# Kernel tuning notes

Hardware: AMD Instinct MI355X
Metric: run time of the kernel (lower is better)

The kernel has to match this reference:

```python
import jax, jax.numpy as jnp
import numpy as np

B, H, IN, OUT, T = 1024, 1024, 512, 8192, 15
EPS = 1e-5


def setup_inputs() -> dict:
    key = jax.random.key(0)
    ks = jax.random.split(key, 20)
    s = 0.02
    d = {
        'z': jax.random.normal(ks[0], (B, H), jnp.float32),
        'input_length': T,
        # ConvTranspose1d weights, torch layout [in, out, k] == jax 'IOH'
        'cw1': jax.random.normal(ks[1], (H, H, 3), jnp.float32) * s,
        'cb1': jax.random.normal(ks[2], (H,), jnp.float32) * s,
        'cw2': jax.random.normal(ks[3], (H, H, 3), jnp.float32) * s,
        'cb2': jax.random.normal(ks[4], (H,), jnp.float32) * s,
        'cw3': jax.random.normal(ks[5], (H, H, 3), jnp.float32) * s,
        'cb3': jax.random.normal(ks[6], (H,), jnp.float32) * s,
        # BatchNorm1d (eval mode: running stats)
        'bn1_g': jnp.ones((H,), jnp.float32), 'bn1_b': jnp.zeros((H,), jnp.float32),
        'bn1_m': jax.random.normal(ks[7], (H,), jnp.float32) * 0.1,
        'bn1_v': jax.random.uniform(ks[8], (H,), jnp.float32, 0.5, 1.5),
        'bn2_g': jnp.ones((H,), jnp.float32), 'bn2_b': jnp.zeros((H,), jnp.float32),
        'bn2_m': jax.random.normal(ks[9], (H,), jnp.float32) * 0.1,
        'bn2_v': jax.random.uniform(ks[10], (H,), jnp.float32, 0.5, 1.5),
        # GRUCell: weight_ih [3H, IN+H], weight_hh [3H, H]
        'w_ih': jax.random.normal(ks[11], (3 * H, IN + H), jnp.float32) * s,
        'w_hh': jax.random.normal(ks[12], (3 * H, H), jnp.float32) * s,
        'b_ih': jax.random.normal(ks[13], (3 * H,), jnp.float32) * s,
        'b_hh': jax.random.normal(ks[14], (3 * H,), jnp.float32) * s,
        # Linears (torch layout [out_features, in_features])
        'h2x_w': jax.random.normal(ks[15], (IN, H), jnp.float32) * s,
        'h2x_b': jax.random.normal(ks[16], (IN,), jnp.float32) * s,
        'dec2out_w': jax.random.normal(ks[17], (OUT, H), jnp.float32) * s,
        'dec2out_b': jnp.zeros((OUT,), jnp.float32),
        'out_w': jax.random.normal(ks[18], (OUT, H), jnp.float32) * s,
        'out_b': jnp.zeros((OUT,), jnp.float32),
    }
    return d


def _conv_t(x, w, b):
    # x: [B, C, L] ; torch ConvTranspose1d(k=3, s=2, pad=0): out L -> 2L+1
    y = jax.lax.conv_transpose(x, w, strides=(2,), padding='VALID',
                               dimension_numbers=('NCH', 'IOH', 'NCH'),
                               transpose_kernel=True)
    return y + b[None, :, None]


def _bn(x, g, bta, m, v):
    inv = g / jnp.sqrt(v + EPS)
    return (x - m[None, :, None]) * inv[None, :, None] + bta[None, :, None]


def reference(z, input_length, cw1, cb1, cw2, cb2, cw3, cb3,
              bn1_g, bn1_b, bn1_m, bn1_v, bn2_g, bn2_b, bn2_m, bn2_v,
              w_ih, w_hh, b_ih, b_hh, h2x_w, h2x_b,
              dec2out_w, dec2out_b, out_w, out_b):
    b = z.shape[0]
    # conv-transpose context: [B, H, 1] -> [B, H, 15]
    dec = z[:, :, None]
    dec = _bn(jax.nn.elu(_conv_t(dec, cw1, cb1)), bn1_g, bn1_b, bn1_m, bn1_v)
    dec = _bn(jax.nn.elu(_conv_t(dec, cw2, cb2)), bn2_g, bn2_b, bn2_m, bn2_v)
    dec = _conv_t(dec, cw3, cb3)
    dec_tbh = jnp.transpose(dec, (2, 0, 1))[:input_length]  # [T, B, H]

    inp0 = jnp.full((b, IN), float(OUT - 2), z.dtype)

    def step(carry, dec_t):
        h, inp = carry
        x = jnp.concatenate([inp, dec_t], axis=1)         # [B, IN+H]
        gi = x @ w_ih.T + b_ih
        gh = h @ w_hh.T + b_hh
        ir, iz, inn = jnp.split(gi, 3, axis=1)
        hr, hz, hn = jnp.split(gh, 3, axis=1)
        r = jax.nn.sigmoid(ir + hr)
        zg = jax.nn.sigmoid(iz + hz)
        n = jnp.tanh(inn + r * hn)
        h_new = (1.0 - zg) * n + zg * h
        inp_new = jax.nn.relu(h_new @ h2x_w.T + h2x_b)    # eval-mode branch
        return (h_new, inp_new), h_new

    (_, _), hs = jax.lax.scan(step, (z, inp0), dec_tbh)   # hs: [T, B, H]

    dec_flat = dec_tbh.reshape(-1, H)
    out_flat = hs.reshape(-1, H)
    dec_o = dec_flat @ dec2out_w.T + dec2out_b            # [T*B, OUT]
    output = out_flat @ out_w.T + out_b                   # [T*B, OUT]
    return output, dec_o
```

## Files before the change

### kernel.cpp

```cpp
#include <hip/hip_runtime.h>
#include <math.h>


#define HD    1024
#define BATCH 1024
#define IND   512
#define OUTD  8192
#define TSTEPS 15
#define EPSV  1e-5f

typedef unsigned short u16;
typedef __attribute__((ext_vector_type(8))) short bf16x8;
typedef __attribute__((ext_vector_type(8))) unsigned short u16x8;
typedef __attribute__((ext_vector_type(4))) unsigned short u16x4;
typedef __attribute__((ext_vector_type(4))) float f32x4;

__device__ __forceinline__ u16 f2b(float f) {
    union { float f; unsigned u; } x; x.f = f;
    unsigned r = x.u + 0x7fffu + ((x.u >> 16) & 1u);
    return (u16)(r >> 16);
}
__device__ __forceinline__ float b2f(u16 v) {
    union { unsigned u; float f; } x; x.u = ((unsigned)v) << 16; return x.f;
}

typedef __attribute__((address_space(1))) const void gas_t;
typedef __attribute__((address_space(3))) void las_t;
__device__ __forceinline__ void gload_lds16(const u16* g, u16* l) {
    __builtin_amdgcn_global_load_lds((gas_t*)g, (las_t*)l, 16, 0, 0);
}

template<int EPI, bool WF32, bool WB16>
__device__ __forceinline__ void gemm_tile128(
    u16* As, u16* Bs,
    int bm, int bn,
    int K1, const u16* A1, int lda1, const u16* B1, int ldb1,
    int K2, const u16* A2, int lda2, const u16* B2, int ldb2,
    const float* bias,
    const float* bng, const float* bnb, const float* bnm, const float* bnv,
    float* Cf, u16* Cb, int ldc)
{
    const int tid  = threadIdx.x;
    const int lane = tid & 63;
    const int w    = tid >> 6;
    const int wr   = w >> 1, wc = w & 1;
    const int r_in = lane >> 2;
    const int c_in = (lane & 3) * 8;

    f32x4 acc[4][4];
#pragma unroll
    for (int m = 0; m < 4; ++m)
#pragma unroll
        for (int n = 0; n < 4; ++n) acc[m][n] = (f32x4){0.f, 0.f, 0.f, 0.f};

#pragma unroll 1
    for (int pair = 0; pair < 2; ++pair) {
        const int K = pair ? K2 : K1;
        if (K == 0) continue;
        const int lda = pair ? lda2 : lda1;
        const int ldb = pair ? ldb2 : ldb1;
        const u16* Ag = (pair ? A2 : A1) + (size_t)bm * lda;
        const u16* Bg = (pair ? B2 : B1) + (size_t)bn * ldb;

        for (int k0 = 0; k0 < K; k0 += 32) {
#pragma unroll
            for (int i = 0; i < 2; ++i) {
                gload_lds16(Ag + (size_t)(i * 64 + w * 16 + r_in) * lda + k0 + c_in,
                            &As[i * 2048 + w * 512]);
                gload_lds16(Bg + (size_t)(i * 64 + w * 16 + r_in) * ldb + k0 + c_in,
                            &Bs[i * 2048 + w * 512]);
            }
            __syncthreads();

            const int fr = lane & 15;
            const int fk = (lane >> 4) * 8;
            bf16x8 av[4], bv[4];
#pragma unroll
            for (int m = 0; m < 4; ++m)
                av[m] = *(const bf16x8*)&As[(wr * 64 + m * 16 + fr) * 32 + fk];
#pragma unroll
            for (int n = 0; n < 4; ++n)
                bv[n] = *(const bf16x8*)&Bs[(wc * 64 + n * 16 + fr) * 32 + fk];
#pragma unroll
            for (int m = 0; m < 4; ++m)
#pragma unroll
                for (int n = 0; n < 4; ++n)
                    acc[m][n] = __builtin_amdgcn_mfma_f32_16x16x32_bf16(
                                    av[m], bv[n], acc[m][n], 0, 0, 0);
            __syncthreads();
        }
    }

    const int col_l = lane & 15;
    const int row_h = (lane >> 4) * 4;
#pragma unroll
    for (int m = 0; m < 4; ++m) {
#pragma unroll
        for (int j = 0; j < 4; ++j) {
            const int row = bm + wr * 64 + m * 16 + row_h + j;
#pragma unroll
            for (int n = 0; n < 4; ++n) {
                const int col = bn + wc * 64 + n * 16 + col_l;
                float v = acc[m][n][j] + bias[col];
                if (EPI == 1) {
                    float e = v > 0.f ? v : expm1f(v);
                    float sc = bng[col] * rsqrtf(bnv[col] + EPSV);
                    v = (e - bnm[col]) * sc + bnb[col];
                }
                if (WF32) Cf[(size_t)row * ldc + col] = v;
                if (WB16) Cb[(size_t)row * ldc + col] = f2b(v);
            }
        }
    }
}

__device__ __forceinline__ void proj_rider(u16* sm, int g,
    const u16* A, const u16* B, const float* bias, float* C)
{
    gemm_tile128<0, true, false>(sm, sm + 4096,
        (g >> 6) * 128, (g & 63) * 128,
        HD, A, HD, B, HD, 0, nullptr, 0, nullptr, 0,
        bias, nullptr, nullptr, nullptr, nullptr, C, nullptr, OUTD);
}

template<int EPI>
__launch_bounds__(256)
__global__ void conv_gemm(int Lin, const u16* X, const u16* W, const float* bias,
                          const float* bng, const float* bnb, const float* bnm, const float* bnv,
                          u16* Y)
{
    __shared__ __align__(16) u16 sm[8192];
    const int t = blockIdx.z;
    int l0 = 0, k0 = 0, l1 = 0, k1 = 0, cnt = 0;
    for (int l = 0; l < Lin; ++l) {
        int k = t - 2 * l;
        if (k >= 0 && k < 3) { if (!cnt) { l0 = l; k0 = k; } else { l1 = l; k1 = k; } ++cnt; }
    }
    const size_t BH = (size_t)BATCH * HD, HH = (size_t)HD * HD;
    gemm_tile128<EPI, false, true>(sm, sm + 4096,
        blockIdx.y * 128, blockIdx.x * 128,
        HD, X + l0 * BH, HD, W + k0 * HH, HD,
        cnt > 1 ? HD : 0, X + l1 * BH, HD, W + k1 * HH, HD,
        bias, bng, bnb, bnm, bnv, nullptr, Y + (size_t)t * BH, HD);
}

__launch_bounds__(512, 2)
__global__ void gemm256(int nbn, int nk,
    const u16* __restrict__ A, const u16* __restrict__ B,
    const float* __restrict__ bias, u16* __restrict__ Cb,
    int lda, int ldb, int ldc)
{
    const int nwg = gridDim.x;
    const int q = nwg >> 3, r = nwg & 7;
    const int xcd = blockIdx.x & 7, idx = blockIdx.x >> 3;
    const int wg = (xcd < r ? xcd * (q + 1) : r * (q + 1) + (xcd - r) * q) + idx;
    int bm, bn;
    const int nbm = nwg / nbn;
    if ((nbn & 3) == 0 && (nbm & 1) == 0) {
        const int nsc = nbn >> 2;
        const int super = wg >> 3, inner = wg & 7;
        const int sr = super / nsc, sc = super - sr * nsc;
        bm = (sr * 2 + (inner >> 2)) * 256;
        bn = (sc * 4 + (inner & 3)) * 256;
    } else {
        bm = (wg / nbn) * 256;
        bn = (wg % nbn) * 256;
    }

    __shared__ __align__(16) u16 smem[2][2][256 * 64];
    u16 (*As)[256 * 64] = smem[0];
    u16 (*Bs)[256 * 64] = smem[1];

    const int tid = threadIdx.x;
    const int w = tid >> 6, l = tid & 63;
    const int wr = w >> 2, wc = w & 3;
    const int srow = l >> 3;
    const int scb  = (l & 7) ^ srow;
    const int fr = l & 15, fcb = l >> 4, swz = l & 7;

    const u16* Ag = A + (size_t)bm * lda;
    const u16* Bg = B + (size_t)bn * ldb;

    auto stage = [&](int b, int kt) {
        const int k0 = kt * 64 + scb * 8;
#pragma unroll
        for (int rr = 0; rr < 4; ++rr)
            gload_lds16(Ag + (size_t)(rr * 64 + w * 8 + srow) * lda + k0,
                        &As[b][(rr * 64 + w * 8) * 64]);
#pragma unroll
        for (int rr = 0; rr < 4; ++rr)
            gload_lds16(Bg + (size_t)(rr * 64 + w * 8 + srow) * ldb + k0,
                        &Bs[b][(rr * 64 + w * 8) * 64]);
    };

    f32x4 acc[8][4];
#pragma unroll
    for (int m = 0; m < 8; ++m)
#pragma unroll
        for (int n = 0; n < 4; ++n) acc[m][n] = (f32x4){0.f, 0.f, 0.f, 0.f};

    stage(0, 0);
    asm volatile("s_waitcnt vmcnt(0)" ::: "memory");
    asm volatile("s_barrier" ::: "memory");

    for (int kt = 0; kt < nk; ++kt) {
        const int c = kt & 1;
        if (kt + 1 < nk) stage(c ^ 1, kt + 1);
#pragma unroll
        for (int ks = 0; ks < 2; ++ks) {
            bf16x8 av[8], bv[4];
#pragma unroll
            for (int m = 0; m < 8; ++m)
                av[m] = *(const bf16x8*)&As[c][
                    (wr * 128 + m * 16 + fr) * 64 + (((ks * 4 + fcb) ^ swz) * 8)];
#pragma unroll
            for (int n = 0; n < 4; ++n)
                bv[n] = *(const bf16x8*)&Bs[c][
                    (wc * 64 + n * 16 + fr) * 64 + (((ks * 4 + fcb) ^ swz) * 8)];
            __builtin_amdgcn_s_setprio(1);
#pragma unroll
            for (int m = 0; m < 8; ++m)
#pragma unroll
                for (int n = 0; n < 4; ++n)
                    acc[m][n] = __builtin_amdgcn_mfma_f32_16x16x32_bf16(
                                    av[m], bv[n], acc[m][n], 0, 0, 0);
            __builtin_amdgcn_s_setprio(0);
        }
        asm volatile("s_waitcnt vmcnt(0)" ::: "memory");
        asm volatile("s_barrier" ::: "memory");
    }

    float* fsm = (float*)smem;
    const int row_h = (l >> 4) * 4;
#pragma unroll 1
    for (int hh = 0; hh < 2; ++hh) {
        __syncthreads();
        if (wr == hh) {
#pragma unroll
            for (int m = 0; m < 8; ++m)
#pragma unroll
                for (int j = 0; j < 4; ++j) {
                    const int rl = m * 16 + row_h + j;
#pragma unroll
                    for (int n = 0; n < 4; ++n)
                        fsm[rl * 256 + wc * 64 + n * 16 + fr] = acc[m][n][j];
                }
        }
        __syncthreads();
#pragma unroll
        for (int it = 0; it < 16; ++it) {
            const int fid = it * 512 + tid;
            const int rl = fid >> 6;
            const int cf = (fid & 63) * 4;
            float4 v = *(const float4*)&fsm[rl * 256 + cf];
            v.x += bias[bn + cf + 0];
            v.y += bias[bn + cf + 1];
            v.z += bias[bn + cf + 2];
            v.w += bias[bn + cf + 3];
            u16x4 o;
            o[0] = f2b(v.x); o[1] = f2b(v.y); o[2] = f2b(v.z); o[3] = f2b(v.w);
            *(u16x4*)&Cb[(size_t)(bm + hh * 128 + rl) * ldc + bn + cf] = o;
        }
    }
}

#define KTILE(Ag, lda_, Bg, ldb_, k0_, ACC2)                                      \
  {                                                                               \
    const int k0 = (k0_);                                                         \
    gload_lds16((Ag) + (size_t)(tid >> 2) * (lda_) + k0 + (tid & 3) * 8,          \
                &As[tid * 8]);                                                    \
    _Pragma("unroll")                                                             \
    for (int i_ = 0; i_ < 3; ++i_) {                                              \
      const int u_ = tid + i_ * 256;                                              \
      gload_lds16((Bg) + (size_t)((u_ >> 8) * HD + bn + ((u_ & 255) >> 2)) * (ldb_)\
                       + k0 + (u_ & 3) * 8,                                       \
                  &Bs[u_ * 8]);                                                   \
    }                                                                             \
    __syncthreads();                                                              \
    {                                                                             \
      bf16x8 av0 = *(const bf16x8*)&As[(wr * 32 + fr) * 32 + fk];                 \
      bf16x8 av1 = *(const bf16x8*)&As[(wr * 32 + 16 + fr) * 32 + fk];            \
      _Pragma("unroll")                                                           \
      for (int n_ = 0; n_ < 2; ++n_) {                                            \
        const int bo = (wc * 32 + n_ * 16 + fr) * 32 + fk;                        \
        bf16x8 bv = *(const bf16x8*)&Bs[bo];                                      \
        ar[0][n_] = __builtin_amdgcn_mfma_f32_16x16x32_bf16(av0, bv, ar[0][n_], 0, 0, 0); \
        ar[1][n_] = __builtin_amdgcn_mfma_f32_16x16x32_bf16(av1, bv, ar[1][n_], 0, 0, 0); \
        bv = *(const bf16x8*)&Bs[2048 + bo];                                      \
        az[0][n_] = __builtin_amdgcn_mfma_f32_16x16x32_bf16(av0, bv, az[0][n_], 0, 0, 0); \
        az[1][n_] = __builtin_amdgcn_mfma_f32_16x16x32_bf16(av1, bv, az[1][n_], 0, 0, 0); \
        bv = *(const bf16x8*)&Bs[4096 + bo];                                      \
        ACC2[0][n_] = __builtin_amdgcn_mfma_f32_16x16x32_bf16(av0, bv, ACC2[0][n_], 0, 0, 0); \
        ACC2[1][n_] = __builtin_amdgcn_mfma_f32_16x16x32_bf16(av1, bv, ACC2[1][n_], 0, 0, 0); \
      }                                                                           \
    }                                                                             \
    __syncthreads();                                                              \
  }

__launch_bounds__(256)
__global__ void gih_cell(int t,
    const u16* __restrict__ inpb,  const u16* __restrict__ wih,
    const u16* __restrict__ hbp,   const u16* __restrict__ whh,
    const u16* __restrict__ gdect, const float* __restrict__ extra0,
    const float* __restrict__ b_hh, const float* __restrict__ hp,
    float* __restrict__ hf, u16* __restrict__ hsbt,
    const u16* __restrict__ dec3b, const u16* __restrict__ d2owb,
    const float* __restrict__ d2ob, float* __restrict__ out1)
{
    __shared__ __align__(16) u16 sm[8192];
    const int bid = blockIdx.x;
    const int tid = threadIdx.x, l = tid & 63, w = tid >> 6;
    const int wr = w >> 1, wc = w & 1;
    const int fr = l & 15, fk = (l >> 4) * 8;

    if (bid >= 256) {
        proj_rider(sm, t * 512 + (bid - 256), dec3b, d2owb, d2ob, out1);
        return;
    }

    u16* As = sm;
    u16* Bs = sm + 2048;
    const int bm = (bid >> 4) * 64;
    const int bn = (bid & 15) * 64;

    f32x4 ar[2][2], az[2][2], ain[2][2], ahn[2][2];
#pragma unroll
    for (int m = 0; m < 2; ++m)
#pragma unroll
        for (int n = 0; n < 2; ++n) {
            ar[m][n] = (f32x4){0.f, 0.f, 0.f, 0.f};
            az[m][n] = (f32x4){0.f, 0.f, 0.f, 0.f};
            ain[m][n] = (f32x4){0.f, 0.f, 0.f, 0.f};
            ahn[m][n] = (f32x4){0.f, 0.f, 0.f, 0.f};
        }

    const u16* Ah = hbp + (size_t)bm * HD;
    const u16* Ai = inpb + (size_t)bm * IND;
    for (int kt = 0; kt < 32; ++kt)
        KTILE(Ah, HD, whh, HD, kt * 32, ahn);
    if (t > 0)
        for (int kt = 0; kt < 16; ++kt)
            KTILE(Ai, IND, wih, (IND + HD), kt * 32, ain);

    const int rh = (l >> 4) * 4;
#pragma unroll
    for (int m = 0; m < 2; ++m)
#pragma unroll
        for (int n = 0; n < 2; ++n)
#pragma unroll
            for (int j = 0; j < 4; ++j) {
                const int R = bm + wr * 32 + m * 16 + rh + j;
                const int C = bn + wc * 32 + n * 16 + fr;
                const size_t g3 = (size_t)R * (3 * HD);
                float gr  = ar[m][n][j] + b2f(gdect[g3 + C])      + b_hh[C];
                float gz  = az[m][n][j] + b2f(gdect[g3 + HD + C]) + b_hh[HD + C];
                float gin = ain[m][n][j] + b2f(gdect[g3 + 2 * HD + C]);
                float ghn = ahn[m][n][j] + b_hh[2 * HD + C];
                if (extra0) {
                    gr  += extra0[C];
                    gz  += extra0[HD + C];
                    gin += extra0[2 * HD + C];
                }
                const float rg = 1.f / (1.f + expf(-gr));
                const float zg = 1.f / (1.f + expf(-gz));
                const float nn = tanhf(gin + rg * ghn);
                const float h  = (1.f - zg) * nn + zg * hp[(size_t)R * HD + C];
                hf[(size_t)R * HD + C] = h;
                hsbt[(size_t)R * HD + C] = f2b(h);
            }
}

__launch_bounds__(256)
__global__ void h2x_k(int t,
    const u16* __restrict__ hbp, const u16* __restrict__ wx,
    const float* __restrict__ xb, u16* __restrict__ inp,
    const u16* __restrict__ hsb, const u16* __restrict__ outwb,
    const float* __restrict__ outb, float* __restrict__ out0)
{
    __shared__ __align__(16) u16 sm[8192];
    const int bid = blockIdx.x;
    const int tid = threadIdx.x, l = tid & 63, w = tid >> 6;
    const int wr = w >> 1, wc = w & 1;
    const int fr = l & 15, fk = (l >> 4) * 8;

    if (bid >= 128) {
        proj_rider(sm, (t - 1) * 512 + (bid - 128), hsb, outwb, outb, out0);
        return;
    }

    u16* As = sm;
    u16* Bs = sm + 2048;
    const int bm = (bid >> 3) * 64;
    const int bn = (bid & 7) * 64;

    f32x4 acc[2][2];
#pragma unroll
    for (int m = 0; m < 2; ++m)
#pragma unroll
        for (int n = 0; n < 2; ++n) acc[m][n] = (f32x4){0.f, 0.f, 0.f, 0.f};
    const u16* Ag = hbp + (size_t)bm * HD;
    const u16* Bg = wx + (size_t)bn * HD;
    for (int kt = 0; kt < 32; ++kt) {
        const int k0 = kt * 32;
        gload_lds16(Ag + (size_t)(tid >> 2) * HD + k0 + (tid & 3) * 8, &As[tid * 8]);
        gload_lds16(Bg + (size_t)(tid >> 2) * HD + k0 + (tid & 3) * 8, &Bs[tid * 8]);
        __syncthreads();
        bf16x8 av0 = *(const bf16x8*)&As[(wr * 32 + fr) * 32 + fk];
        bf16x8 av1 = *(const bf16x8*)&As[(wr * 32 + 16 + fr) * 32 + fk];
#pragma unroll
        for (int n = 0; n < 2; ++n) {
            bf16x8 bv = *(const bf16x8*)&Bs[(wc * 32 + n * 16 + fr) * 32 + fk];
            acc[0][n] = __builtin_amdgcn_mfma_f32_16x16x32_bf16(av0, bv, acc[0][n], 0, 0, 0);
            acc[1][n] = __builtin_amdgcn_mfma_f32_16x16x32_bf16(av1, bv, acc[1][n], 0, 0, 0);
        }
        __syncthreads();
    }
    const int rh = (l >> 4) * 4;
#pragma unroll
    for (int m = 0; m < 2; ++m)
#pragma unroll
        for (int n = 0; n < 2; ++n)
#pragma unroll
            for (int j = 0; j < 4; ++j) {
                const int R = bm + wr * 32 + m * 16 + rh + j;
                const int C = bn + wc * 32 + n * 16 + fr;
                inp[(size_t)R * IND + C] = f2b(fmaxf(acc[m][n][j] + xb[C], 0.f));
            }
}

__launch_bounds__(256)
__global__ void proj_k(int g0, const u16* __restrict__ A, const u16* __restrict__ B,
                       const float* __restrict__ bias, float* __restrict__ C)
{
    __shared__ __align__(16) u16 sm[8192];
    proj_rider(sm, g0 + blockIdx.x, A, B, bias, C);
}

__global__ void pack_w(const float* __restrict__ cw, u16* __restrict__ wp)
{
    __shared__ float lds[768];
    const int o = blockIdx.x, t = threadIdx.x;
    const float* src = cw + (size_t)o * (HD * 3);
    for (int i0 = 0; i0 < HD; i0 += 256) {
#pragma unroll
        for (int r = 0; r < 3; ++r) lds[t + 256 * r] = src[i0 * 3 + t + 256 * r];
        __syncthreads();
#pragma unroll
        for (int k = 0; k < 3; ++k)
            wp[(size_t)k * HD * HD + (size_t)o * HD + i0 + t] = f2b(lds[t * 3 + k]);
        __syncthreads();
    }
}

__global__ void f32_to_b16(const float* __restrict__ s, u16* __restrict__ d, int n)
{
    int i = (blockIdx.x * 256 + threadIdx.x) * 8;
    if (i >= n) return;
    float4 a = *(const float4*)(s + i);
    float4 b = *(const float4*)(s + i + 4);
    u16x8 o;
    o[0] = f2b(a.x); o[1] = f2b(a.y); o[2] = f2b(a.z); o[3] = f2b(a.w);
    o[4] = f2b(b.x); o[5] = f2b(b.y); o[6] = f2b(b.z); o[7] = f2b(b.w);
    *(u16x8*)(d + i) = o;
}

__global__ void ext0_k(const float* __restrict__ w_ih, float* __restrict__ e0)
{
    const int j = blockIdx.x, lane = threadIdx.x;
    float s = 0.f;
    for (int k = lane; k < IND; k += 64) s += w_ih[(size_t)j * (IND + HD) + k];
    for (int off = 32; off; off >>= 1) s += __shfl_down(s, off);
    if (lane == 0) e0[j] = 8190.f * s;
}

extern "C" void kernel_launch(void* const* d_in, const int* in_sizes, int n_in,
                              void* d_out, int out_size, void* d_ws, size_t ws_size,
                              hipStream_t stream)
{
    (void)in_sizes; (void)n_in; (void)out_size; (void)ws_size;

    const float* z    = (const float*)d_in[0];
    const float* cw1  = (const float*)d_in[2];
    const float* cb1  = (const float*)d_in[3];
    const float* cw2  = (const float*)d_in[4];
    const float* cb2  = (const float*)d_in[5];
    const float* cw3  = (const float*)d_in[6];
    const float* cb3  = (const float*)d_in[7];
    const float* bn1g = (const float*)d_in[8];
    const float* bn1b = (const float*)d_in[9];
    const float* bn1m = (const float*)d_in[10];
    const float* bn1v = (const float*)d_in[11];
    const float* bn2g = (const float*)d_in[12];
    const float* bn2b = (const float*)d_in[13];
    const float* bn2m = (const float*)d_in[14];
    const float* bn2v = (const float*)d_in[15];
    const float* w_ih = (const float*)d_in[16];
    const float* w_hh = (const float*)d_in[17];
    const float* b_ih = (const float*)d_in[18];
    const float* b_hh = (const float*)d_in[19];
    const float* h2xw = (const float*)d_in[20];
    const float* h2xb = (const float*)d_in[21];
    const float* d2ow = (const float*)d_in[22];
    const float* d2ob = (const float*)d_in[23];
    const float* outw = (const float*)d_in[24];
    const float* outb = (const float*)d_in[25];

    const size_t HH = (size_t)HD * HD, BH = (size_t)BATCH * HD;
    const size_t B3H = (size_t)BATCH * 3 * HD;

    u16* wsb = (u16*)d_ws;
    size_t off = 0;
    auto A16 = [&](size_t n) { u16* p = wsb + off; off += n; return p; };
    u16* wp1   = A16(3 * HH);
    u16* wp2   = A16(3 * HH);
    u16* wp3   = A16(3 * HH);
    u16* wihb  = A16((size_t)3 * HD * (IND + HD));
    u16* whhb  = A16(3 * HH);
    u16* h2xbw = A16((size_t)IND * HD);
    u16* outwb = A16((size_t)OUTD * HD);
    u16* d2owb = A16((size_t)OUTD * HD);
    u16* zb    = A16(BH);
    u16* decab = A16(3 * BH);
    u16* decbb = A16(7 * BH);
    u16* dec3b = A16(15 * BH);
    u16* hsb   = A16(15 * BH);
    u16* inpb  = A16((size_t)BATCH * IND);
    u16* gdecb = A16((size_t)TSTEPS * B3H);
    float* wsf = (float*)(wsb + ((off + 1) & ~(size_t)1));
    size_t foff = 0;
    auto A32 = [&](size_t n) { float* p = wsf + foff; foff += n; return p; };
    float* h0f   = A32(BH);
    float* h1f   = A32(BH);
    float* extra0= A32(3 * HD);

    pack_w<<<HD, 256, 0, stream>>>(cw1, wp1);
    pack_w<<<HD, 256, 0, stream>>>(cw2, wp2);
    pack_w<<<HD, 256, 0, stream>>>(cw3, wp3);
    auto cvt = [&](const float* s, u16* d, size_t n) {
        f32_to_b16<<<(unsigned)(n / 2048), 256, 0, stream>>>(s, d, (int)n);
    };
    cvt(z, zb, BH);
    cvt(w_ih, wihb, (size_t)3 * HD * (IND + HD));
    cvt(w_hh, whhb, 3 * HH);
    cvt(h2xw, h2xbw, (size_t)IND * HD);
    cvt(outw, outwb, (size_t)OUTD * HD);
    cvt(d2ow, d2owb, (size_t)OUTD * HD);
    ext0_k<<<3 * HD, 64, 0, stream>>>(w_ih, extra0);

    conv_gemm<1><<<dim3(8, 8, 3), 256, 0, stream>>>(1, zb, wp1, cb1,
        bn1g, bn1b, bn1m, bn1v, decab);
    conv_gemm<1><<<dim3(8, 8, 7), 256, 0, stream>>>(3, decab, wp2, cb2,
        bn2g, bn2b, bn2m, bn2v, decbb);
    conv_gemm<0><<<dim3(8, 8, 15), 256, 0, stream>>>(7, decbb, wp3, cb3,
        nullptr, nullptr, nullptr, nullptr, dec3b);

    gemm256<<<dim3((TSTEPS * BATCH / 256) * (3 * HD / 256)), 512, 0, stream>>>(
        3 * HD / 256, HD / 64,
        dec3b, wihb + IND, b_ih, gdecb, HD, IND + HD, 3 * HD);

    float* out0 = (float*)d_out;
    float* out1 = out0 + (size_t)TSTEPS * BATCH * OUTD;
    for (int t = 0; t < TSTEPS; ++t) {
        const u16* hbp   = t ? hsb + (size_t)(t - 1) * BH : zb;
        const float* hpf = (t == 0) ? z : (((t - 1) & 1) ? h1f : h0f);
        float* hwf = (t & 1) ? h1f : h0f;
        if (t > 0)
            h2x_k<<<640, 256, 0, stream>>>(t, hbp, h2xbw, h2xb, inpb,
                hsb, outwb, outb, out0);
        gih_cell<<<768, 256, 0, stream>>>(t,
            inpb, wihb, hbp, whhb, gdecb + (size_t)t * B3H,
            t ? nullptr : extra0, b_hh, hpf, hwf, hsb + (size_t)t * BH,
            dec3b, d2owb, d2ob, out1);
    }
    proj_k<<<512, 256, 0, stream>>>(14 * 512, hsb, outwb, outb, out0);
}
```

Before: 1.537 ms.

## Double-buffer GRU GEMM tiles, rebalance rider projection blocks, batch setup kernels

```diff
diff --git a/kernel.cpp b/kernel.cpp
--- a/kernel.cpp
+++ b/kernel.cpp
@@ -264,37 +264,25 @@
     }
 }
 
-#define KTILE(Ag, lda_, Bg, ldb_, k0_, ACC2)                                      \
+#define GIH_BODY(TGT)                                                             \
   {                                                                               \
-    const int k0 = (k0_);                                                         \
-    gload_lds16((Ag) + (size_t)(tid >> 2) * (lda_) + k0 + (tid & 3) * 8,          \
-                &As[tid * 8]);                                                    \
+    const u16* as = &As[buf * 2048];                                              \
+    const u16* bs = &Bs[buf * 6144];                                              \
+    bf16x8 av0 = *(const bf16x8*)&as[(wr * 32 + fr) * 32 + fk];                   \
+    bf16x8 av1 = *(const bf16x8*)&as[(wr * 32 + 16 + fr) * 32 + fk];              \
     _Pragma("unroll")                                                             \
-    for (int i_ = 0; i_ < 3; ++i_) {                                              \
-      const int u_ = tid + i_ * 256;                                              \
-      gload_lds16((Bg) + (size_t)((u_ >> 8) * HD + bn + ((u_ & 255) >> 2)) * (ldb_)\
-                       + k0 + (u_ & 3) * 8,                                       \
-                  &Bs[u_ * 8]);                                                   \
+    for (int n_ = 0; n_ < 2; ++n_) {                                              \
+      const int bo = (wc * 32 + n_ * 16 + fr) * 32 + fk;                          \
+      bf16x8 bv = *(const bf16x8*)&bs[bo];                                        \
+      ar[0][n_] = __builtin_amdgcn_mfma_f32_16x16x32_bf16(av0, bv, ar[0][n_], 0, 0, 0); \
+      ar[1][n_] = __builtin_amdgcn_mfma_f32_16x16x32_bf16(av1, bv, ar[1][n_], 0, 0, 0); \
+      bv = *(const bf16x8*)&bs[2048 + bo];                                        \
+      az[0][n_] = __builtin_amdgcn_mfma_f32_16x16x32_bf16(av0, bv, az[0][n_], 0, 0, 0); \
+      az[1][n_] = __builtin_amdgcn_mfma_f32_16x16x32_bf16(av1, bv, az[1][n_], 0, 0, 0); \
+      bv = *(const bf16x8*)&bs[4096 + bo];                                        \
+      TGT[0][n_] = __builtin_amdgcn_mfma_f32_16x16x32_bf16(av0, bv, TGT[0][n_], 0, 0, 0); \
+      TGT[1][n_] = __builtin_amdgcn_mfma_f32_16x16x32_bf16(av1, bv, TGT[1][n_], 0, 0, 0); \
     }                                                                             \
-    __syncthreads();                                                              \
-    {                                                                             \
-      bf16x8 av0 = *(const bf16x8*)&As[(wr * 32 + fr) * 32 + fk];                 \
-      bf16x8 av1 = *(const bf16x8*)&As[(wr * 32 + 16 + fr) * 32 + fk];            \
-      _Pragma("unroll")                                                           \
-      for (int n_ = 0; n_ < 2; ++n_) {                                            \
-        const int bo = (wc * 32 + n_ * 16 + fr) * 32 + fk;                        \
-        bf16x8 bv = *(const bf16x8*)&Bs[bo];                                      \
-        ar[0][n_] = __builtin_amdgcn_mfma_f32_16x16x32_bf16(av0, bv, ar[0][n_], 0, 0, 0); \
-        ar[1][n_] = __builtin_amdgcn_mfma_f32_16x16x32_bf16(av1, bv, ar[1][n_], 0, 0, 0); \
-        bv = *(const bf16x8*)&Bs[2048 + bo];                                      \
-        az[0][n_] = __builtin_amdgcn_mfma_f32_16x16x32_bf16(av0, bv, az[0][n_], 0, 0, 0); \
-        az[1][n_] = __builtin_amdgcn_mfma_f32_16x16x32_bf16(av1, bv, az[1][n_], 0, 0, 0); \
-        bv = *(const bf16x8*)&Bs[4096 + bo];                                      \
-        ACC2[0][n_] = __builtin_amdgcn_mfma_f32_16x16x32_bf16(av0, bv, ACC2[0][n_], 0, 0, 0); \
-        ACC2[1][n_] = __builtin_amdgcn_mfma_f32_16x16x32_bf16(av1, bv, ACC2[1][n_], 0, 0, 0); \
-      }                                                                           \
-    }                                                                             \
-    __syncthreads();                                                              \
   }
 
 __launch_bounds__(256)
@@ -307,19 +295,19 @@
     const u16* __restrict__ dec3b, const u16* __restrict__ d2owb,
     const float* __restrict__ d2ob, float* __restrict__ out1)
 {
-    __shared__ __align__(16) u16 sm[8192];
+    __shared__ __align__(16) u16 sm[16384];
     const int bid = blockIdx.x;
     const int tid = threadIdx.x, l = tid & 63, w = tid >> 6;
     const int wr = w >> 1, wc = w & 1;
     const int fr = l & 15, fk = (l >> 4) * 8;
 
     if (bid >= 256) {
-        proj_rider(sm, t * 512 + (bid - 256), dec3b, d2owb, d2ob, out1);
+        proj_rider(sm, t * 384 + (bid - 256), dec3b, d2owb, d2ob, out1);
         return;
     }
 
     u16* As = sm;
-    u16* Bs = sm + 2048;
+    u16* Bs = sm + 4096;
     const int bm = (bid >> 4) * 64;
     const int bn = (bid & 15) * 64;
 
@@ -336,11 +324,42 @@
 
     const u16* Ah = hbp + (size_t)bm * HD;
     const u16* Ai = inpb + (size_t)bm * IND;
-    for (int kt = 0; kt < 32; ++kt)
-        KTILE(Ah, HD, whh, HD, kt * 32, ahn);
-    if (t > 0)
-        for (int kt = 0; kt < 16; ++kt)
-            KTILE(Ai, IND, wih, (IND + HD), kt * 32, ain);
+    const int NT = (t > 0) ? 48 : 32;
+
+    auto stage = [&](int buf, int idx) {
+        const u16* Ag; int lda; const u16* Bg; int ldb; int k0;
+        if (idx < 32) { Ag = Ah; lda = HD;  Bg = whh; ldb = HD;       k0 = idx * 32; }
+        else          { Ag = Ai; lda = IND; Bg = wih; ldb = IND + HD; k0 = (idx - 32) * 32; }
+        gload_lds16(Ag + (size_t)(tid >> 2) * lda + k0 + (tid & 3) * 8,
+                    &As[buf * 2048 + tid * 8]);
+#pragma unroll
+        for (int i_ = 0; i_ < 3; ++i_) {
+            const int u_ = tid + i_ * 256;
+            gload_lds16(Bg + (size_t)((u_ >> 8) * HD + bn + ((u_ & 255) >> 2)) * ldb
+                           + k0 + (u_ & 3) * 8,
+                        &Bs[buf * 6144 + u_ * 8]);
+        }
+    };
+
+    stage(0, 0);
+    asm volatile("s_waitcnt vmcnt(0)" ::: "memory");
+    __syncthreads();
+    for (int idx = 0; idx < 32; ++idx) {
+        const int buf = idx & 1;
+        if (idx + 1 < NT) stage(buf ^ 1, idx + 1);
+        GIH_BODY(ahn);
+        asm volatile("s_waitcnt vmcnt(0)" ::: "memory");
+        __syncthreads();
+    }
+    if (t > 0) {
+        for (int idx = 32; idx < 48; ++idx) {
+            const int buf = idx & 1;
+            if (idx + 1 < 48) stage(buf ^ 1, idx + 1);
+            GIH_BODY(ain);
+            asm volatile("s_waitcnt vmcnt(0)" ::: "memory");
+            __syncthreads();
+        }
+    }
 
     const int rh = (l >> 4) * 4;
 #pragma unroll
@@ -375,7 +394,9 @@
     const u16* __restrict__ hbp, const u16* __restrict__ wx,
     const float* __restrict__ xb, u16* __restrict__ inp,
     const u16* __restrict__ hsb, const u16* __restrict__ outwb,
-    const float* __restrict__ outb, float* __restrict__ out0)
+    const float* __restrict__ outb, float* __restrict__ out0,
+    const u16* __restrict__ dec3b, const u16* __restrict__ d2owb,
+    const float* __restrict__ d2ob, float* __restrict__ out1)
 {
     __shared__ __align__(16) u16 sm[8192];
     const int bid = blockIdx.x;
@@ -383,13 +404,17 @@
     const int wr = w >> 1, wc = w & 1;
     const int fr = l & 15, fk = (l >> 4) * 8;
 
+    if (bid >= 640) {
+        proj_rider(sm, 5760 + (t - 1) * 128 + (bid - 640), dec3b, d2owb, d2ob, out1);
+        return;
+    }
     if (bid >= 128) {
         proj_rider(sm, (t - 1) * 512 + (bid - 128), hsb, outwb, outb, out0);
         return;
     }
 
     u16* As = sm;
-    u16* Bs = sm + 2048;
+    u16* Bs = sm + 4096;
     const int bm = (bid >> 3) * 64;
     const int bn = (bid & 7) * 64;
 
@@ -400,19 +425,32 @@
         for (int n = 0; n < 2; ++n) acc[m][n] = (f32x4){0.f, 0.f, 0.f, 0.f};
     const u16* Ag = hbp + (size_t)bm * HD;
     const u16* Bg = wx + (size_t)bn * HD;
+
+    auto stage = [&](int buf, int kt) {
+        const int k0 = kt * 32;
+        gload_lds16(Ag + (size_t)(tid >> 2) * HD + k0 + (tid & 3) * 8,
+                    &As[buf * 2048 + tid * 8]);
+        gload_lds16(Bg + (size_t)(tid >> 2) * HD + k0 + (tid & 3) * 8,
+                    &Bs[buf * 2048 + tid * 8]);
+    };
+
+    stage(0, 0);
+    asm volatile("s_waitcnt vmcnt(0)" ::: "memory");
+    __syncthreads();
     for (int kt = 0; kt < 32; ++kt) {
-        const int k0 = kt * 32;
-        gload_lds16(Ag + (size_t)(tid >> 2) * HD + k0 + (tid & 3) * 8, &As[tid * 8]);
-        gload_lds16(Bg + (size_t)(tid >> 2) * HD + k0 + (tid & 3) * 8, &Bs[tid * 8]);
-        __syncthreads();
-        bf16x8 av0 = *(const bf16x8*)&As[(wr * 32 + fr) * 32 + fk];
-        bf16x8 av1 = *(const bf16x8*)&As[(wr * 32 + 16 + fr) * 32 + fk];
+        const int buf = kt & 1;
+        if (kt + 1 < 32) stage(buf ^ 1, kt + 1);
+        const u16* as = &As[buf * 2048];
+        const u16* bs = &Bs[buf * 2048];
+        bf16x8 av0 = *(const bf16x8*)&as[(wr * 32 + fr) * 32 + fk];
+        bf16x8 av1 = *(const bf16x8*)&as[(wr * 32 + 16 + fr) * 32 + fk];
 #pragma unroll
         for (int n = 0; n < 2; ++n) {
-            bf16x8 bv = *(const bf16x8*)&Bs[(wc * 32 + n * 16 + fr) * 32 + fk];
+            bf16x8 bv = *(const bf16x8*)&bs[(wc * 32 + n * 16 + fr) * 32 + fk];
             acc[0][n] = __builtin_amdgcn_mfma_f32_16x16x32_bf16(av0, bv, acc[0][n], 0, 0, 0);
             acc[1][n] = __builtin_amdgcn_mfma_f32_16x16x32_bf16(av1, bv, acc[1][n], 0, 0, 0);
         }
+        asm volatile("s_waitcnt vmcnt(0)" ::: "memory");
         __syncthreads();
     }
     const int rh = (l >> 4) * 4;
@@ -429,16 +467,24 @@
 }
 
 __launch_bounds__(256)
-__global__ void proj_k(int g0, const u16* __restrict__ A, const u16* __restrict__ B,
-                       const float* __restrict__ bias, float* __restrict__ C)
+__global__ void proj_k(const u16* __restrict__ A0, const u16* __restrict__ B0,
+                       const float* __restrict__ b0, float* __restrict__ C0,
+                       const u16* __restrict__ A1, const u16* __restrict__ B1,
+                       const float* __restrict__ b1, float* __restrict__ C1)
 {
     __shared__ __align__(16) u16 sm[8192];
-    proj_rider(sm, g0 + blockIdx.x, A, B, bias, C);
-}
-
-__global__ void pack_w(const float* __restrict__ cw, u16* __restrict__ wp)
+    const int bid = blockIdx.x;
+    if (bid < 512) proj_rider(sm, 7168 + bid, A0, B0, b0, C0);
+    else           proj_rider(sm, 7552 + (bid - 512), A1, B1, b1, C1);
+}
+
+__global__ void pack_w3(const float* __restrict__ c1, const float* __restrict__ c2,
+                        const float* __restrict__ c3, u16* __restrict__ p1,
+                        u16* __restrict__ p2, u16* __restrict__ p3)
 {
     __shared__ float lds[768];
+    const float* cw = blockIdx.y == 0 ? c1 : (blockIdx.y == 1 ? c2 : c3);
+    u16* wp = blockIdx.y == 0 ? p1 : (blockIdx.y == 1 ? p2 : p3);
     const int o = blockIdx.x, t = threadIdx.x;
     const float* src = cw + (size_t)o * (HD * 3);
     for (int i0 = 0; i0 < HD; i0 += 256) {
@@ -452,8 +498,22 @@
     }
 }
 
-__global__ void f32_to_b16(const float* __restrict__ s, u16* __restrict__ d, int n)
-{
+__global__ void cvt_all(const float* s0, u16* d0, int n0,
+                        const float* s1, u16* d1, int n1,
+                        const float* s2, u16* d2, int n2,
+                        const float* s3, u16* d3, int n3,
+                        const float* s4, u16* d4, int n4,
+                        const float* s5, u16* d5, int n5)
+{
+    const float* s; u16* d; int n;
+    switch (blockIdx.y) {
+        case 0:  s = s0; d = d0; n = n0; break;
+        case 1:  s = s1; d = d1; n = n1; break;
+        case 2:  s = s2; d = d2; n = n2; break;
+        case 3:  s = s3; d = d3; n = n3; break;
+        case 4:  s = s4; d = d4; n = n4; break;
+        default: s = s5; d = d5; n = n5; break;
+    }
     int i = (blockIdx.x * 256 + threadIdx.x) * 8;
     if (i >= n) return;
     float4 a = *(const float4*)(s + i);
@@ -533,18 +593,14 @@
     float* h1f   = A32(BH);
     float* extra0= A32(3 * HD);
 
-    pack_w<<<HD, 256, 0, stream>>>(cw1, wp1);
-    pack_w<<<HD, 256, 0, stream>>>(cw2, wp2);
-    pack_w<<<HD, 256, 0, stream>>>(cw3, wp3);
-    auto cvt = [&](const float* s, u16* d, size_t n) {
-        f32_to_b16<<<(unsigned)(n / 2048), 256, 0, stream>>>(s, d, (int)n);
-    };
-    cvt(z, zb, BH);
-    cvt(w_ih, wihb, (size_t)3 * HD * (IND + HD));
-    cvt(w_hh, whhb, 3 * HH);
-    cvt(h2xw, h2xbw, (size_t)IND * HD);
-    cvt(outw, outwb, (size_t)OUTD * HD);
-    cvt(d2ow, d2owb, (size_t)OUTD * HD);
+    pack_w3<<<dim3(HD, 3), 256, 0, stream>>>(cw1, cw2, cw3, wp1, wp2, wp3);
+    cvt_all<<<dim3(4096, 6), 256, 0, stream>>>(
+        z, zb, (int)BH,
+        w_ih, wihb, 3 * HD * (IND + HD),
+        w_hh, whhb, (int)(3 * HH),
+        h2xw, h2xbw, IND * HD,
+        outw, outwb, OUTD * HD,
+        d2ow, d2owb, OUTD * HD);
     ext0_k<<<3 * HD, 64, 0, stream>>>(w_ih, extra0);
 
     conv_gemm<1><<<dim3(8, 8, 3), 256, 0, stream>>>(1, zb, wp1, cb1,
@@ -565,12 +621,13 @@
         const float* hpf = (t == 0) ? z : (((t - 1) & 1) ? h1f : h0f);
         float* hwf = (t & 1) ? h1f : h0f;
         if (t > 0)
-            h2x_k<<<640, 256, 0, stream>>>(t, hbp, h2xbw, h2xb, inpb,
-                hsb, outwb, outb, out0);
-        gih_cell<<<768, 256, 0, stream>>>(t,
+            h2x_k<<<768, 256, 0, stream>>>(t, hbp, h2xbw, h2xb, inpb,
+                hsb, outwb, outb, out0, dec3b, d2owb, d2ob, out1);
+        gih_cell<<<640, 256, 0, stream>>>(t,
             inpb, wihb, hbp, whhb, gdecb + (size_t)t * B3H,
             t ? nullptr : extra0, b_hh, hpf, hwf, hsb + (size_t)t * BH,
             dec3b, d2owb, d2ob, out1);
     }
-    proj_k<<<512, 256, 0, stream>>>(14 * 512, hsb, outwb, outb, out0);
-}
+    proj_k<<<640, 256, 0, stream>>>(hsb, outwb, outb, out0,
+                                    dec3b, d2owb, d2ob, out1);
+}
```

Result: slower. 1.651 ms (+7.4%).
